# Kernel tuning notes

Hardware: AMD Instinct MI355X
Metric: run time of the kernel (lower is better)

The kernel has to match this reference:

```python
import jax, jax.numpy as jnp
import numpy as np

B, H, W, DIM, NH = 4, 32, 32, 768, 12
HD = DIM // NH  # head_dim = 64


def setup_inputs() -> dict:
    key = jax.random.key(0)
    ks = jax.random.split(key, 12)
    n = lambda i, shape, s=1.0: jax.random.normal(ks[i], shape, jnp.float32) * s
    return {
        "q": n(0, (B, H, W, DIM)),
        "k": n(1, (B, H, W, DIM)),
        "v": n(2, (B, H, W, DIM)),
        # Linear weights stored as (in, out) so y = x @ W + b (equivalent to torch x @ W.T)
        "Wq": n(3, (DIM, DIM), 0.02), "bq": jnp.zeros((DIM,), jnp.float32),
        "Wk": n(4, (DIM, DIM), 0.02), "bk": jnp.zeros((DIM,), jnp.float32),
        "Wv": n(5, (DIM, DIM), 0.02), "bv": jnp.zeros((DIM,), jnp.float32),
        "Wp": n(6, (DIM, DIM), 0.02), "bp": jnp.zeros((DIM,), jnp.float32),
        # decomposed relative position tables: (2*size - 1, head_dim)
        "rel_pos_h": n(7, (2 * H - 1, HD), 0.02),
        "rel_pos_w": n(8, (2 * W - 1, HD), 0.02),
    }


def reference(q, k, v, Wq, bq, Wk, bk, Wv, bv, Wp, bp, rel_pos_h, rel_pos_w):
    scale = HD ** -0.5

    def to_heads(x, Wt, b):
        y = x.reshape(B, H * W, DIM) @ Wt + b          # (B, HW, DIM)
        return y.reshape(B, H * W, NH, HD).transpose(0, 2, 1, 3).reshape(B * NH, H * W, HD)

    qh = to_heads(q, Wq, bq)   # (B*NH, HW, HD)
    kh = to_heads(k, Wk, bk)
    vh = to_heads(v, Wv, bv)

    # scaled dot-product scores
    attn = jnp.einsum('bqd,bkd->bqk', qh * scale, kh)  # (B*NH, HW, HW)

    # decomposed relative position bias (q_size == k_size == input_size, no interpolation)
    idx_h = jnp.arange(H)[:, None] - jnp.arange(H)[None, :] + (H - 1)
    idx_w = jnp.arange(W)[:, None] - jnp.arange(W)[None, :] + (W - 1)
    Rh = rel_pos_h[idx_h]  # (H, H, HD)
    Rw = rel_pos_w[idx_w]  # (W, W, HD)
    rq = qh.reshape(B * NH, H, W, HD)  # unscaled q, as in torch add_decomposed_rel_pos
    rel_h = jnp.einsum('bhwc,hkc->bhwk', rq, Rh)  # (B*NH, H, W, H)
    rel_w = jnp.einsum('bhwc,wkc->bhwk', rq, Rw)  # (B*NH, H, W, W)

    attn = (attn.reshape(B * NH, H, W, H, W)
            + rel_h[:, :, :, :, None]
            + rel_w[:, :, :, None, :]).reshape(B * NH, H * W, H * W)

    attn = jax.nn.softmax(attn, axis=-1)
    x = (attn @ vh).reshape(B, NH, H, W, HD).transpose(0, 2, 3, 1, 4).reshape(B, H, W, DIM)
    return x @ Wp + bp
```

## Files before the change

kernel.cpp:

```cpp
#include <hip/hip_runtime.h>
#include <math.h>

#define DIM  768
#define NH   12
#define HD   64
#define HWN  1024
#define MROWS 4096
#define LOG2E 1.44269504f

typedef __attribute__((ext_vector_type(8))) short short8;
typedef __attribute__((ext_vector_type(4))) float f32x4;
typedef _Float16 h8 __attribute__((ext_vector_type(8)));
typedef _Float16 h2 __attribute__((ext_vector_type(2)));

__device__ __forceinline__ void gl_lds16(const void* g, void* l) {
    __builtin_amdgcn_global_load_lds(
        (const __attribute__((address_space(1))) void*)g,
        (__attribute__((address_space(3))) void*)l, 16, 0, 0);
}

__device__ __forceinline__ float fexp2(float x) {
    float r;
    asm("v_exp_f32 %0, %1" : "=v"(r) : "v"(x));
    return r;
}

__global__ __launch_bounds__(256) void prep_kernel(
    const float* __restrict__ q, const float* __restrict__ k,
    const float* __restrict__ v,
    const float* __restrict__ Wq, const float* __restrict__ Wk,
    const float* __restrict__ Wv, const float* __restrict__ Wp,
    const float* __restrict__ rph, const float* __restrict__ rpw,
    _Float16* __restrict__ WtAll, _Float16* __restrict__ relTg,
    _Float16* __restrict__ xf16)
{
    __shared__ float Ws[64][65];
    const int b = blockIdx.x;
    const int t = threadIdx.x;

    if (b < 576) {
        const int z = b / 144, rem = b - z * 144;
        const int ky = rem / 12, nx = rem - ky * 12;
        const float* W = (z == 0) ? Wq : (z == 1) ? Wk : (z == 2) ? Wv : Wp;
        _Float16* Wt = WtAll + (size_t)z * 589824;
        const int k0 = ky * 64, n0 = nx * 64;
        {
            int r = t >> 2, c4 = (t & 3) * 16;
            #pragma unroll
            for (int u = 0; u < 16; u += 4)
                *(float4*)&Ws[r][c4 + u] = *(const float4*)(W + (size_t)(k0 + r) * DIM + n0 + c4 + u);
        }
        __syncthreads();
        const int n = t >> 2, kseg = (t & 3) * 16;
        h8 h0, h1;
        #pragma unroll
        for (int j = 0; j < 8; ++j) {
            h0[j] = (_Float16)Ws[kseg + j][n];
            h1[j] = (_Float16)Ws[kseg + 8 + j][n];
        }
        size_t base = (size_t)(n0 + n) * DIM + k0 + kseg;
        *(h8*)(Wt + base) = h0;
        *(h8*)(Wt + base + 8) = h1;
    } else if (b == 576) {
        const int row = t >> 1, c0 = (t & 1) * 32;
        const float* src = (row < 63) ? rph + (size_t)row * HD
                         : (row >= 64 && row < 127) ? rpw + (size_t)(row - 64) * HD
                         : nullptr;
        #pragma unroll
        for (int g = 0; g < 4; ++g) {
            h8 o;
            #pragma unroll
            for (int j = 0; j < 8; ++j)
                o[j] = src ? (_Float16)src[c0 + g * 8 + j] : (_Float16)0.0f;
            *(h8*)(relTg + (size_t)row * HD + c0 + g * 8) = o;
        }
    } else {
        const int N8 = MROWS * DIM / 8;
        int i = (b - 577) * 256 + t;
        const int stride = (gridDim.x - 577) * 256;
        for (; i < 3 * N8; i += stride) {
            const int sel = i / N8, j = i - sel * N8;
            const float* src = (sel == 0) ? q : (sel == 1) ? k : v;
            float4 a0 = ((const float4*)src)[j * 2];
            float4 a1 = ((const float4*)src)[j * 2 + 1];
            h8 o = {(_Float16)a0.x, (_Float16)a0.y, (_Float16)a0.z, (_Float16)a0.w,
                    (_Float16)a1.x, (_Float16)a1.y, (_Float16)a1.z, (_Float16)a1.w};
            *(h8*)(xf16 + (size_t)sel * (MROWS * DIM) + (size_t)j * 8) = o;
        }
    }
}

template<int AMODE>
__global__ __launch_bounds__(256, 3) void gemm_mfma_kernel(
    const _Float16* __restrict__ X0, const _Float16* __restrict__ WtAll,
    const float* __restrict__ bias0, const float* __restrict__ bias1,
    const float* __restrict__ bias2,
    void* __restrict__ Y0, void* __restrict__ Y1, void* __restrict__ Y2)
{
    constexpr int MT = (AMODE == 0) ? 128 : 64;
    constexpr int RF = MT / 32;
    __shared__ __align__(16) char smem[MT * 128 + 12 * 1024];
    constexpr int BOFF = MT * 128;

    const int t = threadIdx.x;
    const int w = t >> 6, lane = t & 63;
    const int l15 = lane & 15, l4 = lane >> 4;

    int sel, rb, cb;
    if (AMODE == 0) {
        const int sw = (blockIdx.x & 7) * 96 + (blockIdx.x >> 3);
        sel = sw >> 8;
        const int rem = sw & 255;
        rb = rem >> 3; cb = rem & 7;
    } else {
        const int sw = (blockIdx.x & 7) * 64 + (blockIdx.x >> 3);
        sel = 3;
        rb = sw >> 3; cb = sw & 7;
    }
    const int row0 = rb * MT, col0 = cb * 96;

    const char* Ab = (const char*)(X0 + (AMODE == 0 ? (size_t)sel * (MROWS * DIM) : 0));
    const _Float16* Bt = WtAll + (size_t)sel * 589824;
    const float* bias = (AMODE == 1) ? bias0 : (sel == 0) ? bias0 : (sel == 1) ? bias1 : bias2;

    f32x4 acc[RF][3];
    #pragma unroll
    for (int i = 0; i < RF; ++i)
        #pragma unroll
        for (int j = 0; j < 3; ++j) acc[i][j] = (f32x4){0, 0, 0, 0};

    for (int kt = 0; kt < 12; ++kt) {
        #pragma unroll
        for (int i = 0; i < MT / 32; ++i) {
            const int fi = w * (MT / 32) + i;
            const int row = fi * 8 + (lane >> 3);
            const int srcb = ((lane & 7) * 16) ^ ((row & 7) << 4);
            gl_lds16(Ab + (size_t)(row0 + row) * 1536 + kt * 128 + srcb, smem + fi * 1024);
        }
        #pragma unroll
        for (int it = 0; it < 3; ++it) {
            const int f = it * 4 + w;
            const int ks = f / 6, cf = f % 6;
            const size_t off = (size_t)(col0 + cf * 16 + l15) * 1536 + kt * 128 + ks * 64 + l4 * 16;
            gl_lds16((const char*)Bt + off, smem + BOFF + f * 1024);
        }
        __syncthreads();

        __builtin_amdgcn_s_setprio(1);
        #pragma unroll
        for (int ks = 0; ks < 2; ++ks) {
            h8 b[3];
            #pragma unroll
            for (int cf4 = 0; cf4 < 3; ++cf4) {
                const int fb = ks * 6 + (w & 1) * 3 + cf4;
                b[cf4] = *(const h8*)(smem + BOFF + fb * 1024 + lane * 16);
            }
            #pragma unroll
            for (int rf = 0; rf < RF; ++rf) {
                const int arow = (w >> 1) * (MT / 2) + rf * 16 + l15;
                const int base = arow * 128 + ((ks * 64 + l4 * 16) ^ ((arow & 7) << 4));
                h8 ah = *(const h8*)(smem + base);
                #pragma unroll
                for (int cf4 = 0; cf4 < 3; ++cf4)
                    acc[rf][cf4] = __builtin_amdgcn_mfma_f32_16x16x32_f16(ah, b[cf4], acc[rf][cf4], 0, 0, 0);
            }
        }
        __builtin_amdgcn_s_setprio(0);
        __syncthreads();
    }

    const int wrow0 = row0 + (w >> 1) * (MT / 2);
    const int wcol0 = col0 + (w & 1) * 48;
    #pragma unroll
    for (int cf4 = 0; cf4 < 3; ++cf4) {
        const int c = wcol0 + cf4 * 16 + l15;
        const float bb = bias[c];
        #pragma unroll
        for (int rf = 0; rf < RF; ++rf) {
            #pragma unroll
            for (int reg = 0; reg < 4; ++reg) {
                const int r = wrow0 + rf * 16 + l4 * 4 + reg;
                float y = acc[rf][cf4][reg] + bb;
                if (AMODE == 1) {
                    ((float*)Y0)[(size_t)r * DIM + c] = y;
                } else {
                    _Float16* Yh = (_Float16*)((sel == 0) ? Y0 : (sel == 1) ? Y1 : Y2);
                    size_t base = ((size_t)((r >> 10) * NH + (c >> 6)) * HWN + (r & 1023)) * HD + (c & 63);
                    Yh[base] = (_Float16)y;
                }
            }
        }
    }
}

#define AT_REL   0
#define AT_VT    8704
#define AT_P     25088
#define AT_KB    33280
#define AT_QF    8704
#define AT_RELT  17920
#define AT_PG    17920
#define AT_OF    8704
#define AT_TOTAL 49664

__global__ __launch_bounds__(256, 3) void attn_kernel(
    const _Float16* __restrict__ qh, const _Float16* __restrict__ kh,
    const _Float16* __restrict__ vh, const _Float16* __restrict__ relTg,
    _Float16* __restrict__ aout)
{
    __shared__ __align__(16) char smem[AT_TOTAL];
    const int bid = blockIdx.x;
    const int j   = bid >> 3;
    const int bh  = (bid & 7) * 6 + (j >> 4);
    const int qb  = j & 15;
    const int t  = threadIdx.x;
    const int w  = t >> 6;
    const int lane = t & 63;
    const int l15 = lane & 15, l4 = lane >> 4;

    _Float16* Rel = (_Float16*)(smem + AT_REL);
    _Float16* Qf  = (_Float16*)(smem + AT_QF);

    const int r = t >> 2, dc = (t & 3) * 16;
    {
        const _Float16* qp = qh + ((size_t)bh * HWN + qb * 64 + r) * HD + dc;
        *(short8*)(&Qf[r * 72 + dc])     = *(const short8*)(qp);
        *(short8*)(&Qf[r * 72 + dc + 8]) = *(const short8*)(qp + 8);
        #pragma unroll
        for (int it = 0; it < 4; ++it) {
            const int f = it * 4 + w;
            const int ct = f >> 1, ks = f & 1;
            gl_lds16((const char*)relTg + (ct * 16 + l15) * 128 + ks * 64 + l4 * 16,
                     smem + AT_RELT + f * 1024);
        }
    }
    __syncthreads();

    const _Float16* kb_ = kh + (size_t)bh * HWN * HD;
    const _Float16* vb_ = vh + (size_t)bh * HWN * HD;
    const int key2 = (t & 31) * 2, dgrp = t >> 5;
    short8 rv0, rv1;
#define LOADV(KT) {                                                            \
        const _Float16* vp = vb_ + (size_t)((KT) * 64 + key2) * HD + dgrp * 8; \
        rv0 = *(const short8*)vp; rv1 = *(const short8*)(vp + HD); }
    LOADV(0);

    h8 qf2[2];
    {
        const int qr = w * 16 + l15;
        qf2[0] = *(const h8*)(&Qf[qr * 72 + l4 * 8]);
        qf2[1] = *(const h8*)(&Qf[qr * 72 + 32 + l4 * 8]);
        const _Float16 qs = (_Float16)(0.125f * LOG2E);
        #pragma unroll
        for (int j2 = 0; j2 < 8; ++j2) { qf2[0][j2] *= qs; qf2[1][j2] *= qs; }
    }

    f32x4 pacc[4][2];
    #pragma unroll
    for (int i = 0; i < 4; ++i)
        #pragma unroll
        for (int j2 = 0; j2 < 2; ++j2) pacc[i][j2] = (f32x4){0, 0, 0, 0};
    #pragma unroll
    for (int ks = 0; ks < 2; ++ks) {
        h8 b0 = *(const h8*)(smem + AT_RELT + ((w * 2 + 0) * 2 + ks) * 1024 + lane * 16);
        h8 b1 = *(const h8*)(smem + AT_RELT + ((w * 2 + 1) * 2 + ks) * 1024 + lane * 16);
        #pragma unroll
        for (int rt = 0; rt < 4; ++rt) {
            h8 a = *(const h8*)(&Qf[(rt * 16 + l15) * 72 + ks * 32 + l4 * 8]);
            pacc[rt][0] = __builtin_amdgcn_mfma_f32_16x16x32_f16(a, b0, pacc[rt][0], 0, 0, 0);
            pacc[rt][1] = __builtin_amdgcn_mfma_f32_16x16x32_f16(a, b1, pacc[rt][1], 0, 0, 0);
        }
    }

    __syncthreads();
    _Float16* Pg = (_Float16*)(smem + AT_PG);
    #pragma unroll
    for (int rt = 0; rt < 4; ++rt)
        #pragma unroll
        for (int cb2 = 0; cb2 < 2; ++cb2)
            #pragma unroll
            for (int reg = 0; reg < 4; ++reg)
                Pg[(rt * 16 + l4 * 4 + reg) * 130 + w * 32 + cb2 * 16 + l15] =
                    (_Float16)(pacc[rt][cb2][reg] * LOG2E);
    __syncthreads();

    {
        const int q = t >> 2, kk0 = (t & 3) * 8;
        const int hw = qb * 64 + q;
        const int hq = hw >> 5, wq = hw & 31;
        short8 vh_, vw_;
        #pragma unroll
        for (int j2 = 0; j2 < 8; ++j2) {
            const int kk = kk0 + j2;
            vh_[j2] = *(const short*)&Pg[q * 130 + (hq + 31 - kk)];
            vw_[j2] = *(const short*)&Pg[q * 130 + 64 + (wq + 31 - kk)];
        }
        *(short8*)(&Rel[q * 68 + kk0])      = vh_;
        *(short8*)(&Rel[q * 68 + 32 + kk0]) = vw_;
    }
    __syncthreads();

    const int qrow_bias = w * 16 + l15;
    float rw_[2][4];
    #pragma unroll
    for (int c2 = 0; c2 < 2; ++c2)
        #pragma unroll
        for (int reg = 0; reg < 4; ++reg)
            rw_[c2][reg] = (float)Rel[qrow_bias * 68 + 32 + c2 * 16 + l4 * 4 + reg];

#define STAGEK(KT, BUF) {                                                      \
        _Pragma("unroll")                                                      \
        for (int i2 = 0; i2 < 2; ++i2) {                                       \
            const int f = w * 2 + i2;                                          \
            const int keyk = f * 8 + (lane >> 3);                              \
            const int srcb = ((lane & 7) * 16) ^ ((lane >> 3) << 4);           \
            gl_lds16((const char*)kb_ + (size_t)((KT) * 64 + keyk) * 128 + srcb, \
                     smem + AT_KB + (BUF) * 8192 + f * 1024);                  \
        } }

#define WRITEVT(BUF) {                                                         \
        _Pragma("unroll")                                                      \
        for (int j2 = 0; j2 < 8; ++j2) {                                       \
            const int d = dgrp * 8 + j2;                                       \
            unsigned pk = ((unsigned short)rv0[j2]) |                          \
                          (((unsigned)(unsigned short)rv1[j2]) << 16);         \
            *(unsigned*)(smem + AT_VT + (BUF) * 8192 + d * 128 +               \
                         ((key2 * 2) ^ ((d & 7) << 4))) = pk; } }
    WRITEVT(0);
    STAGEK(0, 0);

    f32x4 acc_o[4] = {{0,0,0,0},{0,0,0,0},{0,0,0,0},{0,0,0,0}};
    float m_ = -INFINITY, lsum = 0.f;
    char* Pw = smem + AT_P + w * 2048;
    const int swzP = (l15 & 7) << 4;

    #pragma unroll 2
    for (int kt = 0; kt < 16; ++kt) {
        const int cur = kt & 1;
        __syncthreads();
        if (kt < 15) { LOADV(kt + 1); STAGEK(kt + 1, cur ^ 1); }

        h2 rhp = *(const h2*)(&Rel[qrow_bias * 68 + kt * 2]);
        const float rh0 = (float)rhp[0];
        const float rh1 = (float)rhp[1];
        f32x4 accs[4];
        #pragma unroll
        for (int ct = 0; ct < 4; ++ct) {
            const float rhc = (ct >> 1) ? rh1 : rh0;
            #pragma unroll
            for (int reg = 0; reg < 4; ++reg)
                accs[ct][reg] = rw_[ct & 1][reg] + rhc;
        }
        __builtin_amdgcn_s_setprio(1);
        #pragma unroll
        for (int ct = 0; ct < 4; ++ct) {
            const int row = ct * 16 + l15;
            const int swzK = (row & 7) << 4;
            #pragma unroll
            for (int ks = 0; ks < 2; ++ks) {
                h8 kfr = *(const h8*)(smem + AT_KB + cur * 8192 + row * 128 +
                                      ((ks * 64 + l4 * 16) ^ swzK));
                accs[ct] = __builtin_amdgcn_mfma_f32_16x16x32_f16(kfr, qf2[ks], accs[ct], 0, 0, 0);
            }
        }
        __builtin_amdgcn_s_setprio(0);

        float mx[4];
        #pragma unroll
        for (int ct = 0; ct < 4; ++ct)
            mx[ct] = fmaxf(fmaxf(accs[ct][0], accs[ct][1]),
                           fmaxf(accs[ct][2], accs[ct][3]));
        float tmax = fmaxf(fmaxf(mx[0], mx[1]), fmaxf(mx[2], mx[3]));

        if (__any(tmax > m_ + 11.5416f)) {
            float tg = fmaxf(tmax, __shfl_xor(tmax, 16));
            tg = fmaxf(tg, __shfl_xor(tg, 32));
            const float mnew = fmaxf(m_, tg);
            const float factor = fexp2(m_ - mnew);
            m_ = mnew;
            lsum *= factor;
            #pragma unroll
            for (int reg = 0; reg < 4; ++reg) {
                const float fr = __shfl(factor, l4 * 4 + reg);
                #pragma unroll
                for (int dt = 0; dt < 4; ++dt) acc_o[dt][reg] *= fr;
            }
        }

        float tsum = 0.f;
        #pragma unroll
        for (int ct = 0; ct < 4; ++ct) {
            float p0 = fexp2(accs[ct][0] - m_);
            float p1 = fexp2(accs[ct][1] - m_);
            float p2 = fexp2(accs[ct][2] - m_);
            float p3 = fexp2(accs[ct][3] - m_);
            tsum += (p0 + p1) + (p2 + p3);
            h2 pa = {(_Float16)p0, (_Float16)p1};
            h2 pb = {(_Float16)p2, (_Float16)p3};
            uint2 pk;
            pk.x = *(unsigned*)&pa;
            pk.y = *(unsigned*)&pb;
            *(uint2*)(Pw + l15 * 128 + ((ct * 32 + l4 * 8) ^ swzP)) = pk;
        }
        lsum += tsum;

        __builtin_amdgcn_s_setprio(1);
        #pragma unroll
        for (int ks = 0; ks < 2; ++ks) {
            h8 pa = *(const h8*)(Pw + l15 * 128 + ((ks * 64 + l4 * 16) ^ swzP));
            #pragma unroll
            for (int dt = 0; dt < 4; ++dt) {
                const int d = dt * 16 + l15;
                h8 vf = *(const h8*)(smem + AT_VT + cur * 8192 + d * 128 +
                                     ((ks * 64 + l4 * 16) ^ ((d & 7) << 4)));
                acc_o[dt] = __builtin_amdgcn_mfma_f32_16x16x32_f16(pa, vf, acc_o[dt], 0, 0, 0);
            }
        }
        __builtin_amdgcn_s_setprio(0);

        if (kt < 15) WRITEVT(cur ^ 1);
    }

    float ltot = lsum + __shfl_xor(lsum, 16);
    ltot += __shfl_xor(ltot, 32);
    const float invl = 1.0f / ltot;
    float linv[4];
    #pragma unroll
    for (int reg = 0; reg < 4; ++reg) linv[reg] = __shfl(invl, l4 * 4 + reg);
    __syncthreads();
    _Float16* Of = (_Float16*)(smem + AT_OF);
    #pragma unroll
    for (int reg = 0; reg < 4; ++reg) {
        const int qloc = w * 16 + l4 * 4 + reg;
        #pragma unroll
        for (int dt = 0; dt < 4; ++dt)
            Of[qloc * 72 + dt * 16 + l15] = (_Float16)(acc_o[dt][reg] * linv[reg]);
    }
    __syncthreads();
    {
        const int b_ = bh / NH, nh = bh % NH;
        _Float16* op = aout + ((size_t)b_ * HWN + qb * 64 + r) * DIM + nh * HD + dc;
        *(short8*)op       = *(const short8*)(&Of[r * 72 + dc]);
        *(short8*)(op + 8) = *(const short8*)(&Of[r * 72 + dc + 8]);
    }
}

extern "C" void kernel_launch(void* const* d_in, const int* in_sizes, int n_in,
                              void* d_out, int out_size, void* d_ws, size_t ws_size,
                              hipStream_t stream) {
    const float* q   = (const float*)d_in[0];
    const float* k   = (const float*)d_in[1];
    const float* v   = (const float*)d_in[2];
    const float* Wq  = (const float*)d_in[3];
    const float* bq  = (const float*)d_in[4];
    const float* Wk  = (const float*)d_in[5];
    const float* bk  = (const float*)d_in[6];
    const float* Wv  = (const float*)d_in[7];
    const float* bv  = (const float*)d_in[8];
    const float* Wp  = (const float*)d_in[9];
    const float* bp  = (const float*)d_in[10];
    const float* rph = (const float*)d_in[11];
    const float* rpw = (const float*)d_in[12];

    float* out = (float*)d_out;
    char*  w0  = (char*)d_ws;

    _Float16* wtAll = (_Float16*)(w0);
    _Float16* relTg = (_Float16*)(w0 + 4718592);
    _Float16* xf16  = (_Float16*)(w0 + 4734976);
    _Float16* aout  = (_Float16*)(w0 + 4734976);
    _Float16* qf16  = (_Float16*)(w0 + 23609344);
    _Float16* kf16  = (_Float16*)(w0 + 29900800);
    _Float16* vf16  = (_Float16*)(w0 + 36192256);

    dim3 blk(256);
    prep_kernel<<<2625, blk, 0, stream>>>(q, k, v, Wq, Wk, Wv, Wp, rph, rpw,
                                          wtAll, relTg, xf16);
    gemm_mfma_kernel<0><<<768, blk, 0, stream>>>(
        xf16, wtAll, bq, bk, bv, qf16, kf16, vf16);
    attn_kernel<<<768, blk, 0, stream>>>(qf16, kf16, vf16, relTg, aout);
    gemm_mfma_kernel<1><<<512, blk, 0, stream>>>(
        aout, wtAll, bp, nullptr, nullptr, out, nullptr, nullptr);
}
```

Measured before the change: 91.23 us.

## Double-buffer GEMM LDS stages and shrink QKV GEMM tile to 64 rows

The GEMM kernel now uses two LDS buffers and issues the global-to-LDS loads for the next K step before computing the current one. This removes the second barrier per iteration and hides load latency behind the MFMA work. The QKV projection drops from 128-row to 64-row tiles, doubling its grid to 1536 blocks, and the launch-bounds occupancy hint is removed. The cost is more blocks, less reuse of the B-tile per block, and a larger LDS footprint per block.

```diff
diff --git a/kernel.cpp b/kernel.cpp
--- a/kernel.cpp
+++ b/kernel.cpp
@@ -91,16 +91,14 @@
 }
 
 template<int AMODE>
-__global__ __launch_bounds__(256, 3) void gemm_mfma_kernel(
+__global__ __launch_bounds__(256) void gemm_mfma_kernel(
     const _Float16* __restrict__ X0, const _Float16* __restrict__ WtAll,
     const float* __restrict__ bias0, const float* __restrict__ bias1,
     const float* __restrict__ bias2,
     void* __restrict__ Y0, void* __restrict__ Y1, void* __restrict__ Y2)
 {
-    constexpr int MT = (AMODE == 0) ? 128 : 64;
-    constexpr int RF = MT / 32;
-    __shared__ __align__(16) char smem[MT * 128 + 12 * 1024];
-    constexpr int BOFF = MT * 128;
+    constexpr int BUFB = 20480;
+    __shared__ __align__(16) char smem[2 * BUFB];
 
     const int t = threadIdx.x;
     const int w = t >> 6, lane = t & 63;
@@ -108,43 +106,52 @@
 
     int sel, rb, cb;
     if (AMODE == 0) {
-        const int sw = (blockIdx.x & 7) * 96 + (blockIdx.x >> 3);
-        sel = sw >> 8;
-        const int rem = sw & 255;
+        const int sw = (blockIdx.x & 7) * 192 + (blockIdx.x >> 3);
+        sel = sw >> 9;
+        const int rem = sw & 511;
         rb = rem >> 3; cb = rem & 7;
     } else {
         const int sw = (blockIdx.x & 7) * 64 + (blockIdx.x >> 3);
         sel = 3;
         rb = sw >> 3; cb = sw & 7;
     }
-    const int row0 = rb * MT, col0 = cb * 96;
+    const int row0 = rb * 64, col0 = cb * 96;
 
     const char* Ab = (const char*)(X0 + (AMODE == 0 ? (size_t)sel * (MROWS * DIM) : 0));
     const _Float16* Bt = WtAll + (size_t)sel * 589824;
     const float* bias = (AMODE == 1) ? bias0 : (sel == 0) ? bias0 : (sel == 1) ? bias1 : bias2;
 
-    f32x4 acc[RF][3];
-    #pragma unroll
-    for (int i = 0; i < RF; ++i)
+    f32x4 acc[2][3];
+    #pragma unroll
+    for (int i = 0; i < 2; ++i)
         #pragma unroll
         for (int j = 0; j < 3; ++j) acc[i][j] = (f32x4){0, 0, 0, 0};
 
+#define GSTAGE(KT, BUF) {                                                      \
+        char* dst = smem + (BUF) * BUFB;                                       \
+        _Pragma("unroll")                                                      \
+        for (int op = w; op < 20; op += 4) {                                   \
+            if (op < 8) {                                                      \
+                const int row = op * 8 + (lane >> 3);                          \
+                const int srcb = ((lane & 7) * 16) ^ ((row & 7) << 4);         \
+                gl_lds16(Ab + (size_t)(row0 + row) * 1536 + (KT) * 128 + srcb, \
+                         dst + op * 1024);                                     \
+            } else {                                                           \
+                const int f = op - 8;                                          \
+                const int ks = f / 6, cf = f % 6;                              \
+                gl_lds16((const char*)Bt + (size_t)(col0 + cf * 16 + l15) * 1536 \
+                         + (KT) * 128 + ks * 64 + l4 * 16,                     \
+                         dst + 8192 + f * 1024);                               \
+            }                                                                  \
+        } }
+
+    GSTAGE(0, 0);
+
+    #pragma unroll 2
     for (int kt = 0; kt < 12; ++kt) {
-        #pragma unroll
-        for (int i = 0; i < MT / 32; ++i) {
-            const int fi = w * (MT / 32) + i;
-            const int row = fi * 8 + (lane >> 3);
-            const int srcb = ((lane & 7) * 16) ^ ((row & 7) << 4);
-            gl_lds16(Ab + (size_t)(row0 + row) * 1536 + kt * 128 + srcb, smem + fi * 1024);
-        }
-        #pragma unroll
-        for (int it = 0; it < 3; ++it) {
-            const int f = it * 4 + w;
-            const int ks = f / 6, cf = f % 6;
-            const size_t off = (size_t)(col0 + cf * 16 + l15) * 1536 + kt * 128 + ks * 64 + l4 * 16;
-            gl_lds16((const char*)Bt + off, smem + BOFF + f * 1024);
-        }
         __syncthreads();
+        if (kt < 11) GSTAGE(kt + 1, (kt + 1) & 1);
+        const char* buf = smem + (kt & 1) * BUFB;
 
         __builtin_amdgcn_s_setprio(1);
         #pragma unroll
@@ -153,30 +160,29 @@
             #pragma unroll
             for (int cf4 = 0; cf4 < 3; ++cf4) {
                 const int fb = ks * 6 + (w & 1) * 3 + cf4;
-                b[cf4] = *(const h8*)(smem + BOFF + fb * 1024 + lane * 16);
-            }
-            #pragma unroll
-            for (int rf = 0; rf < RF; ++rf) {
-                const int arow = (w >> 1) * (MT / 2) + rf * 16 + l15;
+                b[cf4] = *(const h8*)(buf + 8192 + fb * 1024 + lane * 16);
+            }
+            #pragma unroll
+            for (int rf = 0; rf < 2; ++rf) {
+                const int arow = (w >> 1) * 32 + rf * 16 + l15;
                 const int base = arow * 128 + ((ks * 64 + l4 * 16) ^ ((arow & 7) << 4));
-                h8 ah = *(const h8*)(smem + base);
+                h8 ah = *(const h8*)(buf + base);
                 #pragma unroll
                 for (int cf4 = 0; cf4 < 3; ++cf4)
                     acc[rf][cf4] = __builtin_amdgcn_mfma_f32_16x16x32_f16(ah, b[cf4], acc[rf][cf4], 0, 0, 0);
             }
         }
         __builtin_amdgcn_s_setprio(0);
-        __syncthreads();
-    }
-
-    const int wrow0 = row0 + (w >> 1) * (MT / 2);
+    }
+
+    const int wrow0 = row0 + (w >> 1) * 32;
     const int wcol0 = col0 + (w & 1) * 48;
     #pragma unroll
     for (int cf4 = 0; cf4 < 3; ++cf4) {
         const int c = wcol0 + cf4 * 16 + l15;
         const float bb = bias[c];
         #pragma unroll
-        for (int rf = 0; rf < RF; ++rf) {
+        for (int rf = 0; rf < 2; ++rf) {
             #pragma unroll
             for (int reg = 0; reg < 4; ++reg) {
                 const int r = wrow0 + rf * 16 + l4 * 4 + reg;
@@ -476,7 +482,7 @@
     dim3 blk(256);
     prep_kernel<<<2625, blk, 0, stream>>>(q, k, v, Wq, Wk, Wv, Wp, rph, rpw,
                                           wtAll, relTg, xf16);
-    gemm_mfma_kernel<0><<<768, blk, 0, stream>>>(
+    gemm_mfma_kernel<0><<<1536, blk, 0, stream>>>(
         xf16, wtAll, bq, bk, bv, qf16, kf16, vf16);
     attn_kernel<<<768, blk, 0, stream>>>(qf16, kf16, vf16, relTg, aout);
     gemm_mfma_kernel<1><<<512, blk, 0, stream>>>(
```

New measurement: 97.78 us. 1.07x slower.
